# Kernel tuning notes

Measured on AMD Instinct MI355X. Metric: run time of the kernel, lower is better.

Reference implementation:

```python
import jax, jax.numpy as jnp
import numpy as np

LEAKY_SLOPE = 0.2  # PyG GATv2Conv default negative_slope


def gatv2_layer(x, src, dst, Wl, Wr, att, bias, concat):
    """PyG GATv2Conv (eval mode, dropout off, self-loops already in src/dst).
    x: [N, Din]; Wl/Wr: [Din, H*C]; att: [H, C]; bias: [H*C] or [C].
    """
    N = x.shape[0]
    H, C = att.shape
    xl = (x @ Wl).reshape(N, H, C)   # source transform
    xr = (x @ Wr).reshape(N, H, C)   # target transform
    # per-edge GATv2 score: att . leakyrelu(x_l[j] + x_r[i])
    e = jax.nn.leaky_relu(xl[src] + xr[dst], negative_slope=LEAKY_SLOPE)  # [E, H, C]
    score = jnp.einsum('ehc,hc->eh', e, att)                              # [E, H]
    # segment softmax over incoming edges of each dst node
    m = jax.ops.segment_max(score, dst, num_segments=N)                   # [N, H]
    a = jnp.exp(score - m[dst])
    denom = jax.ops.segment_sum(a, dst, num_segments=N)                   # [N, H]
    alpha = a / denom[dst]                                                # [E, H]
    out = jax.ops.segment_sum(xl[src] * alpha[..., None], dst, num_segments=N)  # [N, H, C]
    out = out.reshape(N, H * C) if concat else out.mean(axis=1)
    return out + bias


def setup_inputs() -> dict:
    key = jax.random.key(0)
    ks = jax.random.split(key, 10)
    N, D, E = 20000, 128, 320000
    HID, HEADS, OUT = 64, 8, 32
    x = jax.random.normal(ks[0], (N, D), dtype=jnp.float32)
    edge_index = jax.random.randint(ks[1], (2, E), 0, N)
    glorot = lambda k, shape, fan: jax.random.normal(k, shape, jnp.float32) * (1.0 / np.sqrt(fan))
    W1l = glorot(ks[2], (D, HEADS * HID), D)
    W1r = glorot(ks[3], (D, HEADS * HID), D)
    att1 = glorot(ks[4], (HEADS, HID), HID)
    b1 = jnp.zeros((HEADS * HID,), jnp.float32)
    W2l = glorot(ks[5], (HEADS * HID, 64), HEADS * HID)
    W2r = glorot(ks[6], (HEADS * HID, 64), HEADS * HID)
    att2 = glorot(ks[7], (1, 64), 64)
    b2 = jnp.zeros((64,), jnp.float32)
    Wlin = glorot(ks[8], (64, OUT), 64)
    blin = jnp.zeros((OUT,), jnp.float32)
    return {"x": x, "edge_index": edge_index, "W1l": W1l, "W1r": W1r, "att1": att1,
            "b1": b1, "W2l": W2l, "W2r": W2r, "att2": att2, "b2": b2,
            "Wlin": Wlin, "blin": blin}


def reference(x, edge_index, W1l, W1r, att1, b1, W2l, W2r, att2, b2, Wlin, blin):
    N = x.shape[0]
    loop = jnp.arange(N)
    src = jnp.concatenate([edge_index[0], loop])  # PyG add_self_loops=True
    dst = jnp.concatenate([edge_index[1], loop])
    h = jax.nn.elu(gatv2_layer(x, src, dst, W1l, W1r, att1, b1, concat=True))
    h = jax.nn.elu(gatv2_layer(h, src, dst, W2l, W2r, att2, b2, concat=False))
    return jax.nn.elu(h @ Wlin + blin)
```

## Files before the change

kernel.cpp:

```cpp
#include <hip/hip_runtime.h>
#include <hip/hip_bf16.h>

typedef __attribute__((ext_vector_type(8))) short short8;
typedef __attribute__((ext_vector_type(4))) float floatx4;
typedef __attribute__((ext_vector_type(2))) float float2v;
typedef __attribute__((ext_vector_type(4))) int int4v;
typedef __attribute__((ext_vector_type(2))) int int2v;

__device__ __forceinline__ float b2f(short s) {
    unsigned u = ((unsigned)(unsigned short)s) << 16;
    float f; __builtin_memcpy(&f, &u, 4); return f;
}
__device__ __forceinline__ short f2b(float f) {
    __hip_bfloat16 hb = __float2bfloat16(f);
    unsigned short us; __builtin_memcpy(&us, &hb, 2);
    return (short)us;
}
__device__ __forceinline__ float2v bpair(int p) {
    unsigned ulo = ((unsigned)p) << 16;
    unsigned uhi = ((unsigned)p) & 0xFFFF0000u;
    float flo, fhi;
    __builtin_memcpy(&flo, &ulo, 4);
    __builtin_memcpy(&fhi, &uhi, 4);
    float2v r; r.x = flo; r.y = fhi; return r;
}

__global__ void prep_all(const float* __restrict__ x,
                         const float* __restrict__ W1l, const float* __restrict__ W1r,
                         const float* __restrict__ W2l, const float* __restrict__ W2r,
                         short* __restrict__ xb, short* __restrict__ w1t,
                         short* __restrict__ w2t, int nx,
                         const int* __restrict__ esrc, const int* __restrict__ edst,
                         int E, int N, int* __restrict__ counts, int* __restrict__ srcs) {
    int tid = blockIdx.x * blockDim.x + threadIdx.x;
    int ET = E + N;
    if (tid < ET) {
        int d, s;
        if (tid < E) { d = edst[tid]; s = esrc[tid]; }
        else { d = tid - E; s = d; }
        int pos = atomicAdd(&counts[d], 1);
        if (pos < 64) srcs[(d << 6) + pos] = s;
    }
    int idx = tid;
    if (idx < nx) { xb[idx] = f2b(x[idx]); return; }
    idx -= nx;
    if (idx < 131072) {
        int n = idx >> 7, k = idx & 127;
        float v = (n < 512) ? W1l[k * 512 + n] : W1r[k * 512 + (n - 512)];
        w1t[idx] = f2b(v);
        return;
    }
    idx -= 131072;
    if (idx < 65536) {
        int n = idx >> 9, k = idx & 511;
        float v = (n < 64) ? W2l[k * 64 + n] : W2r[k * 64 + (n - 64)];
        w2t[idx] = f2b(v);
    }
}

__global__ __launch_bounds__(256) void gemm1(const short* __restrict__ A,
                                             const short* __restrict__ Bt,
                                             short* __restrict__ xl1, short* __restrict__ xr1,
                                             int M) {
    __shared__ short As[64 * 136];
    __shared__ short Bs[128 * 136];
    int t = threadIdx.x;
    int w = t >> 6, L = t & 63, q = L >> 4, s = L & 15;
    int M0 = blockIdx.y * 64, N0 = blockIdx.x * 128;
    #pragma unroll
    for (int i = 0; i < 4; ++i) {
        int c = t + i * 256;
        int r = c >> 4, col = (c & 15) * 8;
        int gr = M0 + r;
        short8 v = {};
        if (gr < M) v = *(const short8*)(A + (size_t)gr * 128 + col);
        *(short8*)(&As[r * 136 + col]) = v;
    }
    #pragma unroll
    for (int i = 0; i < 8; ++i) {
        int c = t + i * 256;
        int r = c >> 4, col = (c & 15) * 8;
        short8 v = *(const short8*)(Bt + (size_t)(N0 + r) * 128 + col);
        *(short8*)(&Bs[r * 136 + col]) = v;
    }
    __syncthreads();
    short8 a[4];
    #pragma unroll
    for (int kk = 0; kk < 4; ++kk)
        a[kk] = *(const short8*)(&As[(w * 16 + s) * 136 + kk * 32 + q * 8]);
    floatx4 acc[8] = {};
    #pragma unroll
    for (int tt = 0; tt < 8; ++tt) {
        #pragma unroll
        for (int kk = 0; kk < 4; ++kk) {
            short8 b = *(const short8*)(&Bs[(tt * 16 + s) * 136 + kk * 32 + q * 8]);
            acc[tt] = __builtin_amdgcn_mfma_f32_16x16x32_bf16(a[kk], b, acc[tt], 0, 0, 0);
        }
    }
    __syncthreads();
    #pragma unroll
    for (int tt = 0; tt < 8; ++tt) {
        #pragma unroll
        for (int rg = 0; rg < 4; ++rg) {
            int rl = w * 16 + q * 4 + rg;
            As[rl * 136 + tt * 16 + s] = f2b(acc[tt][rg]);
        }
    }
    __syncthreads();
    short* Cb = (N0 < 512) ? xl1 : xr1;
    int cb = (N0 < 512) ? N0 : N0 - 512;
    #pragma unroll
    for (int i = 0; i < 4; ++i) {
        int c = t + i * 256;
        int r = c >> 4, col = (c & 15) * 8;
        int row = M0 + r;
        if (row < M) {
            short8 v = *(const short8*)(&As[r * 136 + col]);
            *(short8*)(Cb + (size_t)row * 512 + cb + col) = v;
        }
    }
}

__global__ __launch_bounds__(256) void gemm2(const short* __restrict__ A,
                                             const short* __restrict__ Bt,
                                             short* __restrict__ C, int M) {
    __shared__ short As[32 * 72];
    __shared__ short Bs[64 * 72];
    int t = threadIdx.x;
    int w = t >> 6, L = t & 63, q = L >> 4, s = L & 15;
    int rw = (w >> 1) * 16, cw = (w & 1) * 32;
    int M0 = blockIdx.x * 32, N0 = blockIdx.y * 64;
    floatx4 acc[2] = {};
    for (int k0 = 0; k0 < 512; k0 += 64) {
        {
            int r = t >> 3, col = (t & 7) * 8;
            int gr = M0 + r;
            short8 v = {};
            if (gr < M) v = *(const short8*)(A + (size_t)gr * 512 + k0 + col);
            *(short8*)(&As[r * 72 + col]) = v;
        }
        #pragma unroll
        for (int i = 0; i < 2; ++i) {
            int c = t + i * 256;
            int r = c >> 3, col = (c & 7) * 8;
            short8 v = *(const short8*)(Bt + (size_t)(N0 + r) * 512 + k0 + col);
            *(short8*)(&Bs[r * 72 + col]) = v;
        }
        __syncthreads();
        #pragma unroll
        for (int kk = 0; kk < 2; ++kk) {
            short8 a = *(const short8*)(&As[(rw + s) * 72 + kk * 32 + q * 8]);
            #pragma unroll
            for (int tt = 0; tt < 2; ++tt) {
                short8 b = *(const short8*)(&Bs[(cw + tt * 16 + s) * 72 + kk * 32 + q * 8]);
                acc[tt] = __builtin_amdgcn_mfma_f32_16x16x32_bf16(a, b, acc[tt], 0, 0, 0);
            }
        }
        __syncthreads();
    }
    #pragma unroll
    for (int tt = 0; tt < 2; ++tt) {
        #pragma unroll
        for (int rg = 0; rg < 4; ++rg) {
            int rl = rw + q * 4 + rg;
            As[rl * 72 + cw + tt * 16 + s] = f2b(acc[tt][rg]);
        }
    }
    __syncthreads();
    {
        int r = t >> 3, col = (t & 7) * 8;
        int row = M0 + r;
        if (row < M) {
            short8 v = *(const short8*)(&As[r * 72 + col]);
            *(short8*)(C + (size_t)row * 128 + N0 + col) = v;
        }
    }
}

__global__ void gat_l1(const short* __restrict__ xl, const short* __restrict__ xr,
                       const int* __restrict__ counts, const int* __restrict__ srcs,
                       const float* __restrict__ att, const float* __restrict__ bias,
                       short* __restrict__ h1, int Nn) {
    int i = (blockIdx.x * blockDim.x + threadIdx.x) >> 6;
    if (i >= Nn) return;
    int L = threadIdx.x & 63;
    int c0 = L * 8;
    float2v xrv[4], at[4];
    {
        int4v x4 = *(const int4v*)(xr + (size_t)i * 512 + c0);
        #pragma unroll
        for (int c = 0; c < 4; ++c) {
            xrv[c] = bpair(x4[c]);
            at[c].x = att[c0 + 2 * c];
            at[c].y = att[c0 + 2 * c + 1];
        }
    }
    float2v acc[4] = {};
    float dnm = 0.f;
    int k = i << 6;
    int deg = counts[i]; deg = deg > 64 ? 64 : deg;
    int ke = k + deg;
    for (; k + 1 < ke; k += 2) {
        int j0 = srcs[k], j1 = srcs[k + 1];
        int4v a4 = *(const int4v*)(xl + (size_t)j0 * 512 + c0);
        int4v b4 = *(const int4v*)(xl + (size_t)j1 * 512 + c0);
        float2v v0[4], v1[4];
        float2v p0 = {}, p1 = {};
        #pragma unroll
        for (int c = 0; c < 4; ++c) {
            v0[c] = bpair(a4[c]);
            float2v tv = v0[c] + xrv[c];
            p0 += at[c] * __builtin_elementwise_max(tv, 0.2f * tv);
            v1[c] = bpair(b4[c]);
            float2v tw = v1[c] + xrv[c];
            p1 += at[c] * __builtin_elementwise_max(tw, 0.2f * tw);
        }
        float s0 = p0.x + p0.y, s1 = p1.x + p1.y;
        s0 += __shfl_xor(s0, 1, 64); s0 += __shfl_xor(s0, 2, 64); s0 += __shfl_xor(s0, 4, 64);
        s1 += __shfl_xor(s1, 1, 64); s1 += __shfl_xor(s1, 2, 64); s1 += __shfl_xor(s1, 4, 64);
        float e0 = __expf(s0), e1 = __expf(s1);
        dnm += e0 + e1;
        float2v e02; e02.x = e0; e02.y = e0;
        float2v e12; e12.x = e1; e12.y = e1;
        #pragma unroll
        for (int c = 0; c < 4; ++c) {
            acc[c] += e02 * v0[c];
            acc[c] += e12 * v1[c];
        }
    }
    if (k < ke) {
        int j = srcs[k];
        int4v a4 = *(const int4v*)(xl + (size_t)j * 512 + c0);
        float2v v0[4], p0 = {};
        #pragma unroll
        for (int c = 0; c < 4; ++c) {
            v0[c] = bpair(a4[c]);
            float2v tv = v0[c] + xrv[c];
            p0 += at[c] * __builtin_elementwise_max(tv, 0.2f * tv);
        }
        float s0 = p0.x + p0.y;
        s0 += __shfl_xor(s0, 1, 64); s0 += __shfl_xor(s0, 2, 64); s0 += __shfl_xor(s0, 4, 64);
        float e0 = __expf(s0);
        dnm += e0;
        float2v e02; e02.x = e0; e02.y = e0;
        #pragma unroll
        for (int c = 0; c < 4; ++c) acc[c] += e02 * v0[c];
    }
    float inv = 1.f / dnm;
    short8 o8;
    #pragma unroll
    for (int c = 0; c < 4; ++c) {
        float ox = fmaf(acc[c].x, inv, bias[c0 + 2 * c]);
        float oy = fmaf(acc[c].y, inv, bias[c0 + 2 * c + 1]);
        ox = ox > 0.f ? ox : __expf(ox) - 1.f;
        oy = oy > 0.f ? oy : __expf(oy) - 1.f;
        o8[2 * c] = f2b(ox);
        o8[2 * c + 1] = f2b(oy);
    }
    *(short8*)(h1 + (size_t)i * 512 + c0) = o8;
}

__global__ __launch_bounds__(256) void gat_l2_fin(const short* __restrict__ x2,
                        const int* __restrict__ counts, const int* __restrict__ srcs,
                        const float* __restrict__ att, const float* __restrict__ bias,
                        const float* __restrict__ Wlin, const float* __restrict__ blin,
                        float* __restrict__ out, int Nn) {
    __shared__ float Ws[2048];
    __shared__ float bs[32];
    __shared__ float h2s[4][64];
    int t = threadIdx.x;
    for (int idx = t; idx < 2048; idx += 256) Ws[idx] = Wlin[idx];
    if (t < 32) bs[t] = blin[t];
    __syncthreads();
    int w = t >> 6, L = t & 63;
    int i = blockIdx.x * 4 + w;
    if (i >= Nn) return;
    int g = L >> 4;
    int c4 = (L & 15) * 4;
    float2v xrv[2], at[2];
    {
        int2v xv = *(const int2v*)(x2 + (size_t)i * 128 + 64 + c4);
        xrv[0] = bpair(xv.x);
        xrv[1] = bpair(xv.y);
        floatx4 a4 = *(const floatx4*)(att + c4);
        at[0].x = a4[0]; at[0].y = a4[1];
        at[1].x = a4[2]; at[1].y = a4[3];
    }
    float dnm = 0.f;
    float2v acc0 = {}, acc1 = {};
    int kb = i << 6;
    int deg = counts[i]; deg = deg > 64 ? 64 : deg;
    int ke = kb + deg;
    for (int k0 = kb; k0 < ke; k0 += 4) {
        int k = k0 + g;
        bool val = k < ke;
        int j = srcs[val ? k : kb];
        int2v vv = *(const int2v*)(x2 + (size_t)j * 128 + c4);
        float2v v0 = bpair(vv.x), v1 = bpair(vv.y);
        float2v t0 = v0 + xrv[0], t1 = v1 + xrv[1];
        float2v pp = at[0] * __builtin_elementwise_max(t0, 0.2f * t0)
                   + at[1] * __builtin_elementwise_max(t1, 0.2f * t1);
        float p = pp.x + pp.y;
        p += __shfl_xor(p, 1, 64); p += __shfl_xor(p, 2, 64);
        p += __shfl_xor(p, 4, 64); p += __shfl_xor(p, 8, 64);
        float e = val ? __expf(p) : 0.f;
        dnm += e;
        float2v e2; e2.x = e; e2.y = e;
        acc0 += e2 * v0;
        acc1 += e2 * v1;
    }
    #pragma unroll
    for (int m = 16; m <= 32; m <<= 1) {
        dnm += __shfl_xor(dnm, m, 64);
        acc0.x += __shfl_xor(acc0.x, m, 64);
        acc0.y += __shfl_xor(acc0.y, m, 64);
        acc1.x += __shfl_xor(acc1.x, m, 64);
        acc1.y += __shfl_xor(acc1.y, m, 64);
    }
    float inv = 1.f / dnm;
    floatx4 bv = *(const floatx4*)(bias + c4);
    float o0 = fmaf(acc0.x, inv, bv[0]);
    float o1 = fmaf(acc0.y, inv, bv[1]);
    float o2 = fmaf(acc1.x, inv, bv[2]);
    float o3 = fmaf(acc1.y, inv, bv[3]);
    o0 = o0 > 0.f ? o0 : __expf(o0) - 1.f;
    o1 = o1 > 0.f ? o1 : __expf(o1) - 1.f;
    o2 = o2 > 0.f ? o2 : __expf(o2) - 1.f;
    o3 = o3 > 0.f ? o3 : __expf(o3) - 1.f;
    if (L < 16) {
        floatx4 hv; hv[0] = o0; hv[1] = o1; hv[2] = o2; hv[3] = o3;
        *(floatx4*)(&h2s[w][c4]) = hv;
    }
    int oc = L & 31;
    float accl = 0.f;
    #pragma unroll
    for (int kk = 0; kk < 16; ++kk) {
        floatx4 h = *(const floatx4*)(&h2s[w][kk * 4]);
        accl = fmaf(h[0], Ws[(kk * 4 + 0) * 32 + oc], accl);
        accl = fmaf(h[1], Ws[(kk * 4 + 1) * 32 + oc], accl);
        accl = fmaf(h[2], Ws[(kk * 4 + 2) * 32 + oc], accl);
        accl = fmaf(h[3], Ws[(kk * 4 + 3) * 32 + oc], accl);
    }
    if (L < 32) {
        float r = accl + bs[oc];
        r = r > 0.f ? r : __expf(r) - 1.f;
        out[(size_t)i * 32 + oc] = r;
    }
}

extern "C" void kernel_launch(void* const* d_in, const int* in_sizes, int n_in,
                              void* d_out, int out_size, void* d_ws, size_t ws_size,
                              hipStream_t stream) {
    const float* x    = (const float*)d_in[0];
    const int*   ei   = (const int*)d_in[1];
    const float* W1l  = (const float*)d_in[2];
    const float* W1r  = (const float*)d_in[3];
    const float* att1 = (const float*)d_in[4];
    const float* b1   = (const float*)d_in[5];
    const float* W2l  = (const float*)d_in[6];
    const float* W2r  = (const float*)d_in[7];
    const float* att2 = (const float*)d_in[8];
    const float* b2   = (const float*)d_in[9];
    const float* Wlin = (const float*)d_in[10];
    const float* blin = (const float*)d_in[11];

    const int N  = in_sizes[0] / 128;
    const int E  = in_sizes[1] / 2;

    char* w = (char*)d_ws;
    size_t cur = 0;
    auto take = [&](size_t bytes) -> void* {
        void* p = w + cur;
        cur = (cur + bytes + 255) & ~(size_t)255;
        return p;
    };
    int*   counts = (int*)take((size_t)N * 4);
    int*   srcs   = (int*)take((size_t)N * 64 * 4);
    short* xb     = (short*)take((size_t)N * 128 * 2);
    short* w1t    = (short*)take((size_t)1024 * 128 * 2);
    short* w2t    = (short*)take((size_t)128 * 512 * 2);
    short* xl1    = (short*)take((size_t)N * 512 * 2);
    short* xr1    = (short*)take((size_t)N * 512 * 2);
    short* h1     = (short*)take((size_t)N * 512 * 2);
    short* x2     = (short*)take((size_t)N * 128 * 2);

    hipMemsetAsync(counts, 0, (size_t)N * 4, stream);
    int nprep = N * 128 + 131072 + 65536;
    prep_all<<<(nprep + 255) / 256, 256, 0, stream>>>(x, W1l, W1r, W2l, W2r, xb, w1t, w2t,
                                                      N * 128, ei, ei + E, E, N, counts, srcs);

    gemm1<<<dim3(8, (N + 63) / 64), 256, 0, stream>>>(xb, w1t, xl1, xr1, N);
    gat_l1<<<(N + 3) / 4, 256, 0, stream>>>(xl1, xr1, counts, srcs, att1, b1, h1, N);

    gemm2<<<dim3((N + 31) / 32, 2), 256, 0, stream>>>(h1, w2t, x2, N);
    gat_l2_fin<<<(N + 3) / 4, 256, 0, stream>>>(x2, counts, srcs, att2, b2, Wlin, blin,
                                                (float*)d_out, N);
}
```

Baseline: 212.2 us.

## Fuse layer-1 GAT aggregation with layer-2 GEMM via shared-memory h1 tile

Merges the layer-1 attention aggregation kernel and the second GEMM into one 1024-thread kernel. Each block aggregates 16 nodes into a shared-memory h1 tile, then multiplies that tile by W2 with MFMA, splitting K across two wave groups and reducing through LDS. This removes the h1 round trip to global memory (about 20 MB of writes and reads) and one launch. In exchange, every block reloads the full W2 matrix, the grid assumes N is divisible by 16 with no bounds check, and large blocks with heavy LDS use may lower occupancy.

```diff
diff --git a/kernel.cpp b/kernel.cpp
--- a/kernel.cpp
+++ b/kernel.cpp
@@ -121,143 +121,128 @@
     }
 }
 
-__global__ __launch_bounds__(256) void gemm2(const short* __restrict__ A,
-                                             const short* __restrict__ Bt,
-                                             short* __restrict__ C, int M) {
-    __shared__ short As[32 * 72];
-    __shared__ short Bs[64 * 72];
-    int t = threadIdx.x;
-    int w = t >> 6, L = t & 63, q = L >> 4, s = L & 15;
-    int rw = (w >> 1) * 16, cw = (w & 1) * 32;
-    int M0 = blockIdx.x * 32, N0 = blockIdx.y * 64;
-    floatx4 acc[2] = {};
-    for (int k0 = 0; k0 < 512; k0 += 64) {
-        {
-            int r = t >> 3, col = (t & 7) * 8;
-            int gr = M0 + r;
-            short8 v = {};
-            if (gr < M) v = *(const short8*)(A + (size_t)gr * 512 + k0 + col);
-            *(short8*)(&As[r * 72 + col]) = v;
-        }
-        #pragma unroll
-        for (int i = 0; i < 2; ++i) {
-            int c = t + i * 256;
-            int r = c >> 3, col = (c & 7) * 8;
-            short8 v = *(const short8*)(Bt + (size_t)(N0 + r) * 512 + k0 + col);
-            *(short8*)(&Bs[r * 72 + col]) = v;
-        }
-        __syncthreads();
-        #pragma unroll
-        for (int kk = 0; kk < 2; ++kk) {
-            short8 a = *(const short8*)(&As[(rw + s) * 72 + kk * 32 + q * 8]);
-            #pragma unroll
-            for (int tt = 0; tt < 2; ++tt) {
-                short8 b = *(const short8*)(&Bs[(cw + tt * 16 + s) * 72 + kk * 32 + q * 8]);
-                acc[tt] = __builtin_amdgcn_mfma_f32_16x16x32_bf16(a, b, acc[tt], 0, 0, 0);
-            }
-        }
-        __syncthreads();
-    }
-    #pragma unroll
-    for (int tt = 0; tt < 2; ++tt) {
-        #pragma unroll
-        for (int rg = 0; rg < 4; ++rg) {
-            int rl = rw + q * 4 + rg;
-            As[rl * 72 + cw + tt * 16 + s] = f2b(acc[tt][rg]);
-        }
-    }
-    __syncthreads();
-    {
-        int r = t >> 3, col = (t & 7) * 8;
-        int row = M0 + r;
-        if (row < M) {
-            short8 v = *(const short8*)(&As[r * 72 + col]);
-            *(short8*)(C + (size_t)row * 128 + N0 + col) = v;
-        }
-    }
-}
-
-__global__ void gat_l1(const short* __restrict__ xl, const short* __restrict__ xr,
+__global__ __launch_bounds__(1024) void gat1_gemm2(
+                       const short* __restrict__ xl, const short* __restrict__ xr,
                        const int* __restrict__ counts, const int* __restrict__ srcs,
                        const float* __restrict__ att, const float* __restrict__ bias,
-                       short* __restrict__ h1, int Nn) {
-    int i = (blockIdx.x * blockDim.x + threadIdx.x) >> 6;
-    if (i >= Nn) return;
-    int L = threadIdx.x & 63;
-    int c0 = L * 8;
-    float2v xrv[4], at[4];
+                       const short* __restrict__ w2t, short* __restrict__ x2, int Nn) {
+    __shared__ short h1s[16 * 520];
+    __shared__ short Bs[128 * 136];
+    int t = threadIdx.x;
+    int w = t >> 6, L = t & 63;
+    int i = blockIdx.x * 16 + w;
     {
-        int4v x4 = *(const int4v*)(xr + (size_t)i * 512 + c0);
+        int c0 = L * 8;
+        float2v xrv[4], at[4];
+        {
+            int4v x4 = *(const int4v*)(xr + (size_t)i * 512 + c0);
+            #pragma unroll
+            for (int c = 0; c < 4; ++c) {
+                xrv[c] = bpair(x4[c]);
+                at[c].x = att[c0 + 2 * c];
+                at[c].y = att[c0 + 2 * c + 1];
+            }
+        }
+        float2v acc[4] = {};
+        float dnm = 0.f;
+        int k = i << 6;
+        int deg = counts[i]; deg = deg > 64 ? 64 : deg;
+        int ke = k + deg;
+        for (; k + 1 < ke; k += 2) {
+            int j0 = srcs[k], j1 = srcs[k + 1];
+            int4v a4 = *(const int4v*)(xl + (size_t)j0 * 512 + c0);
+            int4v b4 = *(const int4v*)(xl + (size_t)j1 * 512 + c0);
+            float2v v0[4], v1[4];
+            float2v p0 = {}, p1 = {};
+            #pragma unroll
+            for (int c = 0; c < 4; ++c) {
+                v0[c] = bpair(a4[c]);
+                float2v tv = v0[c] + xrv[c];
+                p0 += at[c] * __builtin_elementwise_max(tv, 0.2f * tv);
+                v1[c] = bpair(b4[c]);
+                float2v tw = v1[c] + xrv[c];
+                p1 += at[c] * __builtin_elementwise_max(tw, 0.2f * tw);
+            }
+            float s0 = p0.x + p0.y, s1 = p1.x + p1.y;
+            s0 += __shfl_xor(s0, 1, 64); s0 += __shfl_xor(s0, 2, 64); s0 += __shfl_xor(s0, 4, 64);
+            s1 += __shfl_xor(s1, 1, 64); s1 += __shfl_xor(s1, 2, 64); s1 += __shfl_xor(s1, 4, 64);
+            float e0 = __expf(s0), e1 = __expf(s1);
+            dnm += e0 + e1;
+            float2v e02; e02.x = e0; e02.y = e0;
+            float2v e12; e12.x = e1; e12.y = e1;
+            #pragma unroll
+            for (int c = 0; c < 4; ++c) {
+                acc[c] += e02 * v0[c];
+                acc[c] += e12 * v1[c];
+            }
+        }
+        if (k < ke) {
+            int j = srcs[k];
+            int4v a4 = *(const int4v*)(xl + (size_t)j * 512 + c0);
+            float2v v0[4], p0 = {};
+            #pragma unroll
+            for (int c = 0; c < 4; ++c) {
+                v0[c] = bpair(a4[c]);
+                float2v tv = v0[c] + xrv[c];
+                p0 += at[c] * __builtin_elementwise_max(tv, 0.2f * tv);
+            }
+            float s0 = p0.x + p0.y;
+            s0 += __shfl_xor(s0, 1, 64); s0 += __shfl_xor(s0, 2, 64); s0 += __shfl_xor(s0, 4, 64);
+            float e0 = __expf(s0);
+            dnm += e0;
+            float2v e02; e02.x = e0; e02.y = e0;
+            #pragma unroll
+            for (int c = 0; c < 4; ++c) acc[c] += e02 * v0[c];
+        }
+        float inv = 1.f / dnm;
+        short8 o8;
         #pragma unroll
         for (int c = 0; c < 4; ++c) {
-            xrv[c] = bpair(x4[c]);
-            at[c].x = att[c0 + 2 * c];
-            at[c].y = att[c0 + 2 * c + 1];
-        }
-    }
-    float2v acc[4] = {};
-    float dnm = 0.f;
-    int k = i << 6;
-    int deg = counts[i]; deg = deg > 64 ? 64 : deg;
-    int ke = k + deg;
-    for (; k + 1 < ke; k += 2) {
-        int j0 = srcs[k], j1 = srcs[k + 1];
-        int4v a4 = *(const int4v*)(xl + (size_t)j0 * 512 + c0);
-        int4v b4 = *(const int4v*)(xl + (size_t)j1 * 512 + c0);
-        float2v v0[4], v1[4];
-        float2v p0 = {}, p1 = {};
-        #pragma unroll
-        for (int c = 0; c < 4; ++c) {
-            v0[c] = bpair(a4[c]);
-            float2v tv = v0[c] + xrv[c];
-            p0 += at[c] * __builtin_elementwise_max(tv, 0.2f * tv);
-            v1[c] = bpair(b4[c]);
-            float2v tw = v1[c] + xrv[c];
-            p1 += at[c] * __builtin_elementwise_max(tw, 0.2f * tw);
-        }
-        float s0 = p0.x + p0.y, s1 = p1.x + p1.y;
-        s0 += __shfl_xor(s0, 1, 64); s0 += __shfl_xor(s0, 2, 64); s0 += __shfl_xor(s0, 4, 64);
-        s1 += __shfl_xor(s1, 1, 64); s1 += __shfl_xor(s1, 2, 64); s1 += __shfl_xor(s1, 4, 64);
-        float e0 = __expf(s0), e1 = __expf(s1);
-        dnm += e0 + e1;
-        float2v e02; e02.x = e0; e02.y = e0;
-        float2v e12; e12.x = e1; e12.y = e1;
-        #pragma unroll
-        for (int c = 0; c < 4; ++c) {
-            acc[c] += e02 * v0[c];
-            acc[c] += e12 * v1[c];
-        }
-    }
-    if (k < ke) {
-        int j = srcs[k];
-        int4v a4 = *(const int4v*)(xl + (size_t)j * 512 + c0);
-        float2v v0[4], p0 = {};
-        #pragma unroll
-        for (int c = 0; c < 4; ++c) {
-            v0[c] = bpair(a4[c]);
-            float2v tv = v0[c] + xrv[c];
-            p0 += at[c] * __builtin_elementwise_max(tv, 0.2f * tv);
-        }
-        float s0 = p0.x + p0.y;
-        s0 += __shfl_xor(s0, 1, 64); s0 += __shfl_xor(s0, 2, 64); s0 += __shfl_xor(s0, 4, 64);
-        float e0 = __expf(s0);
-        dnm += e0;
-        float2v e02; e02.x = e0; e02.y = e0;
-        #pragma unroll
-        for (int c = 0; c < 4; ++c) acc[c] += e02 * v0[c];
-    }
-    float inv = 1.f / dnm;
-    short8 o8;
-    #pragma unroll
-    for (int c = 0; c < 4; ++c) {
-        float ox = fmaf(acc[c].x, inv, bias[c0 + 2 * c]);
-        float oy = fmaf(acc[c].y, inv, bias[c0 + 2 * c + 1]);
-        ox = ox > 0.f ? ox : __expf(ox) - 1.f;
-        oy = oy > 0.f ? oy : __expf(oy) - 1.f;
-        o8[2 * c] = f2b(ox);
-        o8[2 * c + 1] = f2b(oy);
-    }
-    *(short8*)(h1 + (size_t)i * 512 + c0) = o8;
+            float ox = fmaf(acc[c].x, inv, bias[c0 + 2 * c]);
+            float oy = fmaf(acc[c].y, inv, bias[c0 + 2 * c + 1]);
+            ox = ox > 0.f ? ox : __expf(ox) - 1.f;
+            oy = oy > 0.f ? oy : __expf(oy) - 1.f;
+            o8[2 * c] = f2b(ox);
+            o8[2 * c + 1] = f2b(oy);
+        }
+        *(short8*)(&h1s[w * 520 + c0]) = o8;
+    }
+    __syncthreads();
+    int q = L >> 4, s = L & 15;
+    int tt = w & 7, kh = w >> 3;
+    floatx4 cacc = {};
+    for (int k0 = 0; k0 < 512; k0 += 128) {
+        #pragma unroll
+        for (int i2 = 0; i2 < 2; ++i2) {
+            int c = t + i2 * 1024;
+            int r = c >> 4, col = (c & 15) * 8;
+            short8 v = *(const short8*)(w2t + (size_t)r * 512 + k0 + col);
+            *(short8*)(&Bs[r * 136 + col]) = v;
+        }
+        __syncthreads();
+        #pragma unroll
+        for (int kk = 0; kk < 2; ++kk) {
+            short8 a = *(const short8*)(&h1s[s * 520 + k0 + kh * 64 + kk * 32 + q * 8]);
+            short8 b = *(const short8*)(&Bs[(tt * 16 + s) * 136 + kh * 64 + kk * 32 + q * 8]);
+            cacc = __builtin_amdgcn_mfma_f32_16x16x32_bf16(a, b, cacc, 0, 0, 0);
+        }
+        __syncthreads();
+    }
+    float* Cp = (float*)Bs;
+    if (kh == 1) {
+        #pragma unroll
+        for (int rg = 0; rg < 4; ++rg)
+            Cp[tt * 256 + (q * 4 + rg) * 16 + s] = cacc[rg];
+    }
+    __syncthreads();
+    if (kh == 0) {
+        #pragma unroll
+        for (int rg = 0; rg < 4; ++rg) {
+            float v = cacc[rg] + Cp[tt * 256 + (q * 4 + rg) * 16 + s];
+            int row = blockIdx.x * 16 + q * 4 + rg;
+            x2[(size_t)row * 128 + tt * 16 + s] = f2b(v);
+        }
+    }
 }
 
 __global__ __launch_bounds__(256) void gat_l2_fin(const short* __restrict__ x2,
@@ -381,7 +366,6 @@
     short* w2t    = (short*)take((size_t)128 * 512 * 2);
     short* xl1    = (short*)take((size_t)N * 512 * 2);
     short* xr1    = (short*)take((size_t)N * 512 * 2);
-    short* h1     = (short*)take((size_t)N * 512 * 2);
     short* x2     = (short*)take((size_t)N * 128 * 2);
 
     hipMemsetAsync(counts, 0, (size_t)N * 4, stream);
@@ -390,9 +374,7 @@
                                                       N * 128, ei, ei + E, E, N, counts, srcs);
 
     gemm1<<<dim3(8, (N + 63) / 64), 256, 0, stream>>>(xb, w1t, xl1, xr1, N);
-    gat_l1<<<(N + 3) / 4, 256, 0, stream>>>(xl1, xr1, counts, srcs, att1, b1, h1, N);
-
-    gemm2<<<dim3((N + 31) / 32, 2), 256, 0, stream>>>(h1, w2t, x2, N);
+    gat1_gemm2<<<N / 16, 1024, 0, stream>>>(xl1, xr1, counts, srcs, att1, b1, w2t, x2, N);
     gat_l2_fin<<<(N + 3) / 4, 256, 0, stream>>>(x2, counts, srcs, att2, b2, Wlin, blin,
                                                 (float*)d_out, N);
 }
```

Result: slower. 224.6 us (+5.8%).

## Fuse fp32-to-bf16 conversion of x into gemm1 and compute two column tiles per block

Applied to the files above, without the earlier changes.

gemm1 now reads x in fp32, converts it to bf16 while staging the A tile in shared memory, and drops the separate xb buffer along with the conversion pass in prep_all. Each block now covers 256 output columns in two sequential 128-column tiles, reusing the A fragment, which halves the grid in x. The aim is to cut the extra read and write of x and the repeated A loads. The cost is a smaller grid with fewer blocks and more work serialized inside each block.

```diff
diff --git a/kernel.cpp b/kernel.cpp
--- a/kernel.cpp
+++ b/kernel.cpp
@@ -2,6 +2,7 @@
 #include <hip/hip_bf16.h>
 
 typedef __attribute__((ext_vector_type(8))) short short8;
+typedef __attribute__((ext_vector_type(4))) short shortx4;
 typedef __attribute__((ext_vector_type(4))) float floatx4;
 typedef __attribute__((ext_vector_type(2))) float float2v;
 typedef __attribute__((ext_vector_type(4))) int int4v;
@@ -25,11 +26,9 @@
     float2v r; r.x = flo; r.y = fhi; return r;
 }
 
-__global__ void prep_all(const float* __restrict__ x,
-                         const float* __restrict__ W1l, const float* __restrict__ W1r,
+__global__ void prep_all(const float* __restrict__ W1l, const float* __restrict__ W1r,
                          const float* __restrict__ W2l, const float* __restrict__ W2r,
-                         short* __restrict__ xb, short* __restrict__ w1t,
-                         short* __restrict__ w2t, int nx,
+                         short* __restrict__ w1t, short* __restrict__ w2t,
                          const int* __restrict__ esrc, const int* __restrict__ edst,
                          int E, int N, int* __restrict__ counts, int* __restrict__ srcs) {
     int tid = blockIdx.x * blockDim.x + threadIdx.x;
@@ -42,8 +41,6 @@
         if (pos < 64) srcs[(d << 6) + pos] = s;
     }
     int idx = tid;
-    if (idx < nx) { xb[idx] = f2b(x[idx]); return; }
-    idx -= nx;
     if (idx < 131072) {
         int n = idx >> 7, k = idx & 127;
         float v = (n < 512) ? W1l[k * 512 + n] : W1r[k * 512 + (n - 512)];
@@ -58,7 +55,7 @@
     }
 }
 
-__global__ __launch_bounds__(256) void gemm1(const short* __restrict__ A,
+__global__ __launch_bounds__(256) void gemm1(const float* __restrict__ X,
                                              const short* __restrict__ Bt,
                                              short* __restrict__ xl1, short* __restrict__ xr1,
                                              int M) {
@@ -66,57 +63,67 @@
     __shared__ short Bs[128 * 136];
     int t = threadIdx.x;
     int w = t >> 6, L = t & 63, q = L >> 4, s = L & 15;
-    int M0 = blockIdx.y * 64, N0 = blockIdx.x * 128;
-    #pragma unroll
-    for (int i = 0; i < 4; ++i) {
-        int c = t + i * 256;
-        int r = c >> 4, col = (c & 15) * 8;
-        int gr = M0 + r;
-        short8 v = {};
-        if (gr < M) v = *(const short8*)(A + (size_t)gr * 128 + col);
-        *(short8*)(&As[r * 136 + col]) = v;
-    }
+    int M0 = blockIdx.y * 64, NB = blockIdx.x * 256;
     #pragma unroll
     for (int i = 0; i < 8; ++i) {
         int c = t + i * 256;
-        int r = c >> 4, col = (c & 15) * 8;
-        short8 v = *(const short8*)(Bt + (size_t)(N0 + r) * 128 + col);
-        *(short8*)(&Bs[r * 136 + col]) = v;
-    }
-    __syncthreads();
+        int r = c >> 5, col = (c & 31) * 4;
+        int gr = M0 + r;
+        floatx4 v = {};
+        if (gr < M) v = *(const floatx4*)(X + (size_t)gr * 128 + col);
+        shortx4 s4;
+        #pragma unroll
+        for (int j = 0; j < 4; ++j) s4[j] = f2b(v[j]);
+        *(shortx4*)(&As[r * 136 + col]) = s4;
+    }
     short8 a[4];
     #pragma unroll
-    for (int kk = 0; kk < 4; ++kk)
-        a[kk] = *(const short8*)(&As[(w * 16 + s) * 136 + kk * 32 + q * 8]);
-    floatx4 acc[8] = {};
-    #pragma unroll
-    for (int tt = 0; tt < 8; ++tt) {
-        #pragma unroll
-        for (int kk = 0; kk < 4; ++kk) {
-            short8 b = *(const short8*)(&Bs[(tt * 16 + s) * 136 + kk * 32 + q * 8]);
-            acc[tt] = __builtin_amdgcn_mfma_f32_16x16x32_bf16(a[kk], b, acc[tt], 0, 0, 0);
-        }
-    }
-    __syncthreads();
-    #pragma unroll
-    for (int tt = 0; tt < 8; ++tt) {
-        #pragma unroll
-        for (int rg = 0; rg < 4; ++rg) {
-            int rl = w * 16 + q * 4 + rg;
-            As[rl * 136 + tt * 16 + s] = f2b(acc[tt][rg]);
-        }
-    }
-    __syncthreads();
-    short* Cb = (N0 < 512) ? xl1 : xr1;
-    int cb = (N0 < 512) ? N0 : N0 - 512;
-    #pragma unroll
-    for (int i = 0; i < 4; ++i) {
-        int c = t + i * 256;
-        int r = c >> 4, col = (c & 15) * 8;
-        int row = M0 + r;
-        if (row < M) {
-            short8 v = *(const short8*)(&As[r * 136 + col]);
-            *(short8*)(Cb + (size_t)row * 512 + cb + col) = v;
+    for (int tile = 0; tile < 2; ++tile) {
+        int N0 = NB + tile * 128;
+        if (tile) __syncthreads();
+        #pragma unroll
+        for (int i = 0; i < 8; ++i) {
+            int c = t + i * 256;
+            int r = c >> 4, col = (c & 15) * 8;
+            short8 v = *(const short8*)(Bt + (size_t)(N0 + r) * 128 + col);
+            *(short8*)(&Bs[r * 136 + col]) = v;
+        }
+        __syncthreads();
+        if (tile == 0) {
+            #pragma unroll
+            for (int kk = 0; kk < 4; ++kk)
+                a[kk] = *(const short8*)(&As[(w * 16 + s) * 136 + kk * 32 + q * 8]);
+        }
+        floatx4 acc[8] = {};
+        #pragma unroll
+        for (int tt = 0; tt < 8; ++tt) {
+            #pragma unroll
+            for (int kk = 0; kk < 4; ++kk) {
+                short8 b = *(const short8*)(&Bs[(tt * 16 + s) * 136 + kk * 32 + q * 8]);
+                acc[tt] = __builtin_amdgcn_mfma_f32_16x16x32_bf16(a[kk], b, acc[tt], 0, 0, 0);
+            }
+        }
+        __syncthreads();
+        #pragma unroll
+        for (int tt = 0; tt < 8; ++tt) {
+            #pragma unroll
+            for (int rg = 0; rg < 4; ++rg) {
+                int rl = w * 16 + q * 4 + rg;
+                Bs[rl * 136 + tt * 16 + s] = f2b(acc[tt][rg]);
+            }
+        }
+        __syncthreads();
+        short* Cb = (N0 < 512) ? xl1 : xr1;
+        int cb = (N0 < 512) ? N0 : N0 - 512;
+        #pragma unroll
+        for (int i = 0; i < 4; ++i) {
+            int c = t + i * 256;
+            int r = c >> 4, col = (c & 15) * 8;
+            int row = M0 + r;
+            if (row < M) {
+                short8 v = *(const short8*)(&Bs[r * 136 + col]);
+                *(short8*)(Cb + (size_t)row * 512 + cb + col) = v;
+            }
         }
     }
 }
@@ -366,6 +373,7 @@
 
     const int N  = in_sizes[0] / 128;
     const int E  = in_sizes[1] / 2;
+    const int ET = E + N;
 
     char* w = (char*)d_ws;
     size_t cur = 0;
@@ -376,7 +384,6 @@
     };
     int*   counts = (int*)take((size_t)N * 4);
     int*   srcs   = (int*)take((size_t)N * 64 * 4);
-    short* xb     = (short*)take((size_t)N * 128 * 2);
     short* w1t    = (short*)take((size_t)1024 * 128 * 2);
     short* w2t    = (short*)take((size_t)128 * 512 * 2);
     short* xl1    = (short*)take((size_t)N * 512 * 2);
@@ -385,11 +392,11 @@
     short* x2     = (short*)take((size_t)N * 128 * 2);
 
     hipMemsetAsync(counts, 0, (size_t)N * 4, stream);
-    int nprep = N * 128 + 131072 + 65536;
-    prep_all<<<(nprep + 255) / 256, 256, 0, stream>>>(x, W1l, W1r, W2l, W2r, xb, w1t, w2t,
-                                                      N * 128, ei, ei + E, E, N, counts, srcs);
-
-    gemm1<<<dim3(8, (N + 63) / 64), 256, 0, stream>>>(xb, w1t, xl1, xr1, N);
+    int nprep = ET > 196608 ? ET : 196608;
+    prep_all<<<(nprep + 255) / 256, 256, 0, stream>>>(W1l, W1r, W2l, W2r, w1t, w2t,
+                                                      ei, ei + E, E, N, counts, srcs);
+
+    gemm1<<<dim3(4, (N + 63) / 64), 256, 0, stream>>>(x, w1t, xl1, xr1, N);
     gat_l1<<<(N + 3) / 4, 256, 0, stream>>>(xl1, xr1, counts, srcs, att1, b1, h1, N);
 
     gemm2<<<dim3((N + 31) / 32, 2), 256, 0, stream>>>(h1, w2t, x2, N);
```

Measured after the change: 213.4 us. No clear change (+0.6%).
